# Kernel tuning notes

Hardware: AMD Instinct MI355X
Metric: run time of the kernel (lower is better)

## Reference

```python
import jax, jax.numpy as jnp
import numpy as np

DIM, ATT, G, T, KL, B = 1024, 128, 8, 4096, 256, 8
GD = DIM // G
SCALE = 1.0 / np.sqrt(ATT)

def setup_inputs() -> dict:
    key = jax.random.key(0)
    ks = jax.random.split(key, 7)
    x = jax.random.normal(ks[0], (B, T, DIM), dtype=jnp.float32)
    # stacked per-group weights (einsum orientation: in_dim x out_dim)
    Wq = jax.random.normal(ks[1], (G, GD, ATT), dtype=jnp.float32) * (1.0 / np.sqrt(GD))
    Wk = jax.random.normal(ks[2], (G, GD, ATT), dtype=jnp.float32) * (1.0 / np.sqrt(GD))
    Wv = jax.random.normal(ks[3], (G, GD, GD), dtype=jnp.float32) * (1.0 / np.sqrt(GD))
    Wo = jax.random.normal(ks[4], (G, GD, GD), dtype=jnp.float32) * (1.0 / np.sqrt(GD))
    Pk = jax.random.normal(ks[5], (G, T, KL), dtype=jnp.float32) * (1.0 / np.sqrt(T))
    Pv = jax.random.normal(ks[6], (G, T, KL), dtype=jnp.float32) * (1.0 / np.sqrt(T))
    return {"x": x, "Wq": Wq, "Wk": Wk, "Wv": Wv, "Wo": Wo, "Pk": Pk, "Pv": Pv}

def reference(x, Wq, Wk, Wv, Wo, Pk, Pv):
    Bx, Tx, _ = x.shape
    xg = x.reshape(Bx, Tx, G, GD).transpose(0, 2, 1, 3)        # [B,G,T,gd]
    q = jnp.einsum('bgtd,gda->bgta', xg, Wq)                   # [B,G,T,att]
    k = jnp.einsum('bgtd,gda->bgta', xg, Wk)
    v = jnp.einsum('bgtd,gde->bgte', xg, Wv)                   # [B,G,T,gd]
    k_red = jnp.einsum('bgta,gtk->bgka', k, Pk)                # [B,G,kl,att]
    v_red = jnp.einsum('bgte,gtk->bgke', v, Pv)                # [B,G,kl,gd]
    att = jax.nn.softmax(jnp.einsum('bgta,bgka->bgtk', q, k_red) * SCALE, axis=-1)
    out = jnp.einsum('bgtk,bgke->bgte', att, v_red)            # [B,G,T,gd]
    out = jnp.einsum('bgte,gef->bgtf', out, Wo)                # per-group output proj
    return out.transpose(0, 2, 1, 3).reshape(Bx, Tx, DIM)      # concat groups on last dim
```

## Files before the change

### kernel.cpp

```cpp
#include <hip/hip_runtime.h>
#include <hip/hip_bf16.h>

#define NB 8
#define NG 8
#define NT 4096
#define NDIM 1024
#define NGD 128
#define NATT 128
#define NKL 256
#define FSCALE 0.08838834764831845f

typedef __bf16 bf16x8 __attribute__((ext_vector_type(8)));
typedef float f32x4 __attribute__((ext_vector_type(4)));
typedef ushort u16x8 __attribute__((ext_vector_type(8)));
typedef ushort u16x4 __attribute__((ext_vector_type(4)));

#define MFMA(a, b, c) __builtin_amdgcn_mfma_f32_16x16x32_bf16(a, b, c, 0, 0, 0)

__device__ __forceinline__ ushort f2bf(float f) {
  union { float f; unsigned u; } v; v.f = f;
  unsigned r = v.u + 0x7FFFu + ((v.u >> 16) & 1u);
  return (ushort)(r >> 16);
}

__device__ __forceinline__ void gload16(const ushort* g, ushort* l) {
  __builtin_amdgcn_global_load_lds(
      (const __attribute__((address_space(1))) unsigned int*)g,
      (__attribute__((address_space(3))) unsigned int*)l, 16, 0, 0);
}

__global__ __launch_bounds__(512) void k0_weights(
    const float* __restrict__ Wq, const float* __restrict__ Wk,
    const float* __restrict__ Wv, const float* __restrict__ Wo,
    ushort* __restrict__ WkQT, ushort* __restrict__ WvoT) {
  const int sel = blockIdx.x;
  const int g = blockIdx.y;
  __shared__ float A2[128 * 136];
  __shared__ float B2[128 * 136];
  const int tid = threadIdx.x;

  if (sel == 0) {
#pragma unroll
    for (int u = 0; u < 8; ++u) {
      const int c = tid + 512 * u;
      const int row = c >> 5, c4 = (c & 31) * 4;
      *(float4*)&A2[row * 136 + c4] =
          *(const float4*)&Wo[(size_t)g * 16384 + row * 128 + c4];
      const float4 v = *(const float4*)&Wv[(size_t)g * 16384 + row * 128 + c4];
      B2[(c4 + 0) * 136 + row] = v.x;
      B2[(c4 + 1) * 136 + row] = v.y;
      B2[(c4 + 2) * 136 + row] = v.z;
      B2[(c4 + 3) * 136 + row] = v.w;
    }
  } else {
#pragma unroll
    for (int u = 0; u < 8; ++u) {
      const int c = tid + 512 * u;
      const int row = c >> 5, c4 = (c & 31) * 4;
      const float4 q = *(const float4*)&Wq[(size_t)g * 16384 + row * 128 + c4];
      A2[(c4 + 0) * 136 + row] = q.x;
      A2[(c4 + 1) * 136 + row] = q.y;
      A2[(c4 + 2) * 136 + row] = q.z;
      A2[(c4 + 3) * 136 + row] = q.w;
      const float4 k = *(const float4*)&Wk[(size_t)g * 16384 + row * 128 + c4];
      B2[(c4 + 0) * 136 + row] = k.x;
      B2[(c4 + 1) * 136 + row] = k.y;
      B2[(c4 + 2) * 136 + row] = k.z;
      B2[(c4 + 3) * 136 + row] = k.w;
    }
  }
  __syncthreads();

  const int mr = tid >> 4;
  const int mc = tid & 15;
  float acc[4][8];
#pragma unroll
  for (int i = 0; i < 4; ++i)
#pragma unroll
    for (int j = 0; j < 8; ++j) acc[i][j] = 0.f;

#pragma unroll 4
  for (int k = 0; k < 128; ++k) {
    const float4 a = *(const float4*)&A2[k * 136 + mr * 4];
    const float4 b0 = *(const float4*)&B2[k * 136 + mc * 8];
    const float4 b1 = *(const float4*)&B2[k * 136 + mc * 8 + 4];
    const float av[4] = {a.x, a.y, a.z, a.w};
    const float bv[8] = {b0.x, b0.y, b0.z, b0.w, b1.x, b1.y, b1.z, b1.w};
#pragma unroll
    for (int i = 0; i < 4; ++i)
#pragma unroll
      for (int j = 0; j < 8; ++j) acc[i][j] += av[i] * bv[j];
  }

  const float sc = sel ? FSCALE : 1.f;
  ushort* dst = (sel ? WkQT : WvoT) + (size_t)g * 16384;
#pragma unroll
  for (int i = 0; i < 4; ++i) {
    u16x8 pk;
#pragma unroll
    for (int j = 0; j < 8; ++j) pk[j] = f2bf(acc[i][j] * sc);
    *(u16x8*)&dst[(size_t)(mr * 4 + i) * 128 + mc * 8] = pk;
  }
}

__global__ __launch_bounds__(256) void kt_x(const float* __restrict__ x,
                                            ushort* __restrict__ xT) {
  const int t0 = blockIdx.x * 64;
  const int bg = blockIdx.y;
  const int b = bg >> 3, g = bg & 7;
  __shared__ float xl[64 * 132];
#pragma unroll
  for (int u = 0; u < 8; ++u) {
    const int c = threadIdx.x + 256 * u;
    const int row = c >> 5, c4 = (c & 31) * 4;
    *(float4*)&xl[row * 132 + c4] =
        *(const float4*)&x[((size_t)b * NT + t0 + row) * NDIM + g * 128 + c4];
  }
  __syncthreads();
  const int seg = threadIdx.x & 7;
  const int d0 = threadIdx.x >> 3;
#pragma unroll
  for (int u = 0; u < 4; ++u) {
    const int d = d0 + u * 32;
    u16x8 pk;
#pragma unroll
    for (int z = 0; z < 8; ++z) pk[z] = f2bf(xl[(seg * 8 + z) * 132 + d]);
    *(u16x8*)&xT[((size_t)bg * 128 + d) * NT + t0 + seg * 8] = pk;
  }
}

__global__ __launch_bounds__(256) void kt_p(const float* __restrict__ P,
                                            ushort* __restrict__ PT) {
  const int t0 = blockIdx.x * 64;
  const int klh = blockIdx.y, g = blockIdx.z;
  __shared__ float pl[64 * 132];
#pragma unroll
  for (int u = 0; u < 8; ++u) {
    const int c = threadIdx.x + 256 * u;
    const int row = c >> 5, c4 = (c & 31) * 4;
    *(float4*)&pl[row * 132 + c4] =
        *(const float4*)&P[((size_t)g * NT + t0 + row) * NKL + klh * 128 + c4];
  }
  __syncthreads();
  const int seg = threadIdx.x & 7;
  const int k0 = threadIdx.x >> 3;
#pragma unroll
  for (int u = 0; u < 4; ++u) {
    const int kl = k0 + u * 32;
    u16x8 pk;
#pragma unroll
    for (int z = 0; z < 8; ++z) pk[z] = f2bf(pl[(seg * 8 + z) * 132 + kl]);
    *(u16x8*)&PT[((size_t)g * NKL + klh * 128 + kl) * NT + t0 + seg * 8] = pk;
  }
}

__global__ __launch_bounds__(256, 2) void k1_mfma(
    const ushort* __restrict__ PkT, const ushort* __restrict__ PvT,
    const ushort* __restrict__ xT, const ushort* __restrict__ WkQT,
    const ushort* __restrict__ WvoT, ushort* __restrict__ MQ,
    ushort* __restrict__ vo_redT) {
  const int bid = blockIdx.x;
  const int work = (bid & 7) * 32 + (bid >> 3);
  const int bg = work >> 2;
  const int sel = (work >> 1) & 1;
  const int klt = work & 1;
  const int g = bg & 7;
  const ushort* PT = (sel ? PvT : PkT) + ((size_t)g * NKL + klt * 128) * NT;
  const ushort* Xb = xT + (size_t)bg * 128 * NT;

  __shared__ ushort lds[17408];

  const int tid = threadIdx.x;
  const int w = tid >> 6, lane = tid & 63;
  const int l15 = lane & 15, l4 = lane >> 4;
  const int rh = (w & 1) * 64;
  const int ch = (w >> 1) * 64;
  const int srow = lane >> 2, sc = lane & 3;

  f32x4 acc[4][4];
  const f32x4 fz = {0.f, 0.f, 0.f, 0.f};
#pragma unroll
  for (int i = 0; i < 4; ++i)
#pragma unroll
    for (int j = 0; j < 4; ++j) acc[i][j] = fz;

#define K1_STAGE(buf, s)                                                     \
  {                                                                          \
    const int t0_ = (s) * 32;                                                \
    ushort* Ab_ = &lds[(buf) * 8192];                                        \
    ushort* Bb_ = &lds[(buf) * 8192 + 4096];                                 \
    _Pragma("unroll") for (int u = 0; u < 2; ++u) {                          \
      const int row_ = w * 32 + u * 16 + srow;                               \
      const size_t off_ = (size_t)row_ * NT + t0_ + ((sc ^ (row_ & 3)) << 3);\
      gload16(PT + off_, Ab_ + (w * 32 + u * 16) * 32);                      \
      gload16(Xb + off_, Bb_ + (w * 32 + u * 16) * 32);                      \
    }                                                                        \
  }

#define K1_COMPUTE(buf)                                                      \
  {                                                                          \
    const ushort* Ab_ = &lds[(buf) * 8192];                                  \
    const ushort* Bb_ = &lds[(buf) * 8192 + 4096];                           \
    bf16x8 af_[4], bf_[4];                                                   \
    _Pragma("unroll") for (int i = 0; i < 4; ++i) {                          \
      const int row_ = rh + i * 16 + l15;                                    \
      af_[i] = *(const bf16x8*)&Ab_[row_ * 32 + ((l4 ^ (row_ & 3)) << 3)];   \
    }                                                                        \
    _Pragma("unroll") for (int j = 0; j < 4; ++j) {                          \
      const int row_ = ch + j * 16 + l15;                                    \
      bf_[j] = *(const bf16x8*)&Bb_[row_ * 32 + ((l4 ^ (row_ & 3)) << 3)];   \
    }                                                                        \
    _Pragma("unroll") for (int i = 0; i < 4; ++i)                            \
      _Pragma("unroll") for (int j = 0; j < 4; ++j)                          \
        acc[i][j] = MFMA(af_[i], bf_[j], acc[i][j]);                         \
  }

  K1_STAGE(0, 0);
  __syncthreads();
  int buf = 0;
#pragma unroll 1
  for (int s = 0; s < 128; ++s) {
    if (s + 1 < 128) K1_STAGE(buf ^ 1, s + 1);
    K1_COMPUTE(buf);
    __syncthreads();
    buf ^= 1;
  }

  ushort* C = lds;
#pragma unroll
  for (int i = 0; i < 4; ++i)
#pragma unroll
    for (int j = 0; j < 4; ++j)
#pragma unroll
      for (int r = 0; r < 4; ++r)
        C[(rh + i * 16 + l4 * 4 + r) * 136 + ch + j * 16 + l15] =
            f2bf(acc[i][j][r]);
  __syncthreads();

  const ushort* WT = (sel ? WvoT : WkQT) + (size_t)g * 16384;
  f32x4 o[4][4];
#pragma unroll
  for (int i = 0; i < 4; ++i)
#pragma unroll
    for (int j = 0; j < 4; ++j) o[i][j] = fz;
#pragma unroll
  for (int ks = 0; ks < 4; ++ks) {
    bf16x8 af[4], bfr[4];
#pragma unroll
    for (int i = 0; i < 4; ++i)
      af[i] = *(const bf16x8*)&C[(rh + i * 16 + l15) * 136 + ks * 32 + l4 * 8];
#pragma unroll
    for (int j = 0; j < 4; ++j)
      bfr[j] = *(const bf16x8*)&WT[(size_t)(ch + j * 16 + l15) * 128 + ks * 32 + l4 * 8];
#pragma unroll
    for (int i = 0; i < 4; ++i)
#pragma unroll
      for (int j = 0; j < 4; ++j) o[i][j] = MFMA(af[i], bfr[j], o[i][j]);
  }

  if (sel == 0) {
#pragma unroll
    for (int i = 0; i < 4; ++i)
#pragma unroll
      for (int j = 0; j < 4; ++j)
#pragma unroll
        for (int r = 0; r < 4; ++r)
          MQ[((size_t)bg * NKL + klt * 128 + rh + i * 16 + l4 * 4 + r) * 128 +
             ch + j * 16 + l15] = f2bf(o[i][j][r]);
  } else {
#pragma unroll
    for (int i = 0; i < 4; ++i)
#pragma unroll
      for (int j = 0; j < 4; ++j) {
        u16x4 pk;
#pragma unroll
        for (int r = 0; r < 4; ++r) pk[r] = f2bf(o[i][j][r]);
        *(u16x4*)&vo_redT[((size_t)bg * 128 + ch + j * 16 + l15) * NKL +
                          klt * 128 + rh + i * 16 + l4 * 4] = pk;
      }
  }
}

__global__ __launch_bounds__(512, 2) void k2_attn(
    const float* __restrict__ x, const ushort* __restrict__ MQ,
    const ushort* __restrict__ vo_redT, float* __restrict__ out) {
  const int tc = blockIdx.x;
  const int bg = blockIdx.y;
  const int b = bg >> 3, g = bg & 7;

  __shared__ ushort mq[256 * 136];
  __shared__ ushort att[64 * 264];
  __shared__ float redm[2][64];
  __shared__ float reds[2][64];

  const int tid = threadIdx.x;
  const int w = tid >> 6, lane = tid & 63;
  const int l15 = lane & 15, l4 = lane >> 4;
  const int tw = w >> 1, half = w & 1;
  const f32x4 fz = {0.f, 0.f, 0.f, 0.f};

  {
    const ushort* src = MQ + (size_t)bg * NKL * 128;
#pragma unroll
    for (int u = 0; u < 8; ++u) {
      const int c = tid + 512 * u;
      const int r = c >> 4, c8 = (c & 15) * 8;
      *(u16x8*)&mq[r * 136 + c8] = *(const u16x8*)&src[r * 128 + c8];
    }
  }

  const float* xb = x + ((size_t)b * NT + tc * 512) * NDIM + g * 128;
  const ushort* vo = vo_redT + ((size_t)bg * 128 + half * 64) * NKL;

  float4 xr[8];
#pragma unroll
  for (int ks = 0; ks < 4; ++ks) {
    const float* p = xb + (size_t)(tw * 16 + l15) * NDIM + ks * 32 + l4 * 8;
    xr[ks * 2] = *(const float4*)p;
    xr[ks * 2 + 1] = *(const float4*)(p + 4);
  }
  __syncthreads();

#pragma unroll 1
  for (int st = 0; st < 8; ++st) {
    bf16x8 a[4];
#pragma unroll
    for (int ks = 0; ks < 4; ++ks) {
      bf16x8 t;
      t[0] = (__bf16)xr[ks * 2].x; t[1] = (__bf16)xr[ks * 2].y;
      t[2] = (__bf16)xr[ks * 2].z; t[3] = (__bf16)xr[ks * 2].w;
      t[4] = (__bf16)xr[ks * 2 + 1].x; t[5] = (__bf16)xr[ks * 2 + 1].y;
      t[6] = (__bf16)xr[ks * 2 + 1].z; t[7] = (__bf16)xr[ks * 2 + 1].w;
      a[ks] = t;
    }
    if (st + 1 < 8) {
      const float* pn = xb + (size_t)((st + 1) * 64 + tw * 16 + l15) * NDIM;
#pragma unroll
      for (int ks = 0; ks < 4; ++ks) {
        xr[ks * 2] = *(const float4*)(pn + ks * 32 + l4 * 8);
        xr[ks * 2 + 1] = *(const float4*)(pn + ks * 32 + l4 * 8 + 4);
      }
    }
    f32x4 s[8];
#pragma unroll
    for (int n = 0; n < 8; ++n) s[n] = fz;
#pragma unroll
    for (int n = 0; n < 8; ++n) {
      const int row = (half * 8 + n) * 16 + l15;
#pragma unroll
      for (int ks = 0; ks < 4; ++ks) {
        const bf16x8 bv = *(const bf16x8*)&mq[row * 136 + ks * 32 + l4 * 8];
        s[n] = MFMA(a[ks], bv, s[n]);
      }
    }
    const int rowbase = tw * 16 + l4 * 4;
    float inv[4];
    {
      float mx[4];
#pragma unroll
      for (int r = 0; r < 4; ++r) {
        float m = s[0][r];
#pragma unroll
        for (int n = 1; n < 8; ++n) m = fmaxf(m, s[n][r]);
#pragma unroll
        for (int off = 1; off < 16; off <<= 1) m = fmaxf(m, __shfl_xor(m, off, 64));
        mx[r] = m;
      }
      if (l15 == 0) {
#pragma unroll
        for (int r = 0; r < 4; ++r) redm[half][rowbase + r] = mx[r];
      }
      __syncthreads();
      float sm[4];
#pragma unroll
      for (int r = 0; r < 4; ++r) {
        const float mg = fmaxf(mx[r], redm[half ^ 1][rowbase + r]);
        float acc = 0.f;
#pragma unroll
        for (int n = 0; n < 8; ++n) {
          const float p = __expf(s[n][r] - mg);
          acc += p;
          att[(rowbase + r) * 264 + (half * 8 + n) * 16 + l15] = f2bf(p);
        }
#pragma unroll
        for (int off = 1; off < 16; off <<= 1) acc += __shfl_xor(acc, off, 64);
        sm[r] = acc;
      }
      if (l15 == 0) {
#pragma unroll
        for (int r = 0; r < 4; ++r) reds[half][rowbase + r] = sm[r];
      }
      __syncthreads();
#pragma unroll
      for (int r = 0; r < 4; ++r)
        inv[r] = 1.f / (sm[r] + reds[half ^ 1][rowbase + r]);
    }
    f32x4 oa[4];
#pragma unroll
    for (int j = 0; j < 4; ++j) oa[j] = fz;
#pragma unroll
    for (int ks = 0; ks < 8; ++ks) {
      const bf16x8 av = *(const bf16x8*)&att[(tw * 16 + l15) * 264 + ks * 32 + l4 * 8];
#pragma unroll
      for (int j = 0; j < 4; ++j) {
        const bf16x8 bv = *(const bf16x8*)&vo[(size_t)(j * 16 + l15) * NKL + ks * 32 + l4 * 8];
        oa[j] = MFMA(av, bv, oa[j]);
      }
    }
    float* ob = out + ((size_t)b * NT + tc * 512 + st * 64 + tw * 16) * NDIM +
                g * 128 + half * 64;
#pragma unroll
    for (int j = 0; j < 4; ++j)
#pragma unroll
      for (int r = 0; r < 4; ++r)
        ob[(size_t)(l4 * 4 + r) * NDIM + j * 16 + l15] = oa[j][r] * inv[r];
  }
}

extern "C" void kernel_launch(void* const* d_in, const int* in_sizes, int n_in,
                              void* d_out, int out_size, void* d_ws, size_t ws_size,
                              hipStream_t stream) {
  (void)in_sizes; (void)n_in; (void)out_size; (void)ws_size;
  const float* x  = (const float*)d_in[0];
  const float* Wq = (const float*)d_in[1];
  const float* Wk = (const float*)d_in[2];
  const float* Wv = (const float*)d_in[3];
  const float* Wo = (const float*)d_in[4];
  const float* Pk = (const float*)d_in[5];
  const float* Pv = (const float*)d_in[6];

  ushort* wsu = (ushort*)d_ws;
  ushort* PkT     = wsu;
  ushort* PvT     = PkT + 8388608;
  ushort* WkQT    = PvT + 8388608;
  ushort* WvoT    = WkQT + 131072;
  ushort* MQ      = WvoT + 131072;
  ushort* vo_redT = MQ + 2097152;
  ushort* xT = (ushort*)d_out;

  k0_weights<<<dim3(2, NG), dim3(512), 0, stream>>>(Wq, Wk, Wv, Wo, WkQT, WvoT);
  kt_x<<<dim3(64, 64), dim3(256), 0, stream>>>(x, xT);
  kt_p<<<dim3(64, 2, 8), dim3(256), 0, stream>>>(Pk, PkT);
  kt_p<<<dim3(64, 2, 8), dim3(256), 0, stream>>>(Pv, PvT);
  k1_mfma<<<dim3(256), dim3(256), 0, stream>>>(PkT, PvT, xT, WkQT, WvoT,
                                               MQ, vo_redT);
  k2_attn<<<dim3(8, 64), dim3(512), 0, stream>>>(x, MQ, vo_redT, (float*)d_out);
}
```

Baseline: 259.6 us.

## Merge transpose kernels into one launch and deepen k1 K-tile to 64

The three transpose/convert kernels for x, Pk and Pv are merged into a single launch that dispatches on block index, removing two launches and their tail gaps. The k1 MFMA GEMM stage doubles its K-step from 32 to 64 per LDS buffer with an 8-way XOR swizzle, halving the number of barriers and loop iterations. The cost is that LDS per block roughly doubles to 64KB, which may limit the two-blocks-per-CU occupancy that launch_bounds requests.

```diff
diff --git a/kernel.cpp b/kernel.cpp
--- a/kernel.cpp
+++ b/kernel.cpp
@@ -103,54 +103,62 @@
   }
 }
 
-__global__ __launch_bounds__(256) void kt_x(const float* __restrict__ x,
-                                            ushort* __restrict__ xT) {
-  const int t0 = blockIdx.x * 64;
-  const int bg = blockIdx.y;
-  const int b = bg >> 3, g = bg & 7;
-  __shared__ float xl[64 * 132];
-#pragma unroll
-  for (int u = 0; u < 8; ++u) {
-    const int c = threadIdx.x + 256 * u;
-    const int row = c >> 5, c4 = (c & 31) * 4;
-    *(float4*)&xl[row * 132 + c4] =
-        *(const float4*)&x[((size_t)b * NT + t0 + row) * NDIM + g * 128 + c4];
-  }
-  __syncthreads();
-  const int seg = threadIdx.x & 7;
-  const int d0 = threadIdx.x >> 3;
-#pragma unroll
-  for (int u = 0; u < 4; ++u) {
-    const int d = d0 + u * 32;
-    u16x8 pk;
-#pragma unroll
-    for (int z = 0; z < 8; ++z) pk[z] = f2bf(xl[(seg * 8 + z) * 132 + d]);
-    *(u16x8*)&xT[((size_t)bg * 128 + d) * NT + t0 + seg * 8] = pk;
-  }
-}
-
-__global__ __launch_bounds__(256) void kt_p(const float* __restrict__ P,
-                                            ushort* __restrict__ PT) {
-  const int t0 = blockIdx.x * 64;
-  const int klh = blockIdx.y, g = blockIdx.z;
-  __shared__ float pl[64 * 132];
-#pragma unroll
-  for (int u = 0; u < 8; ++u) {
-    const int c = threadIdx.x + 256 * u;
-    const int row = c >> 5, c4 = (c & 31) * 4;
-    *(float4*)&pl[row * 132 + c4] =
-        *(const float4*)&P[((size_t)g * NT + t0 + row) * NKL + klh * 128 + c4];
-  }
-  __syncthreads();
-  const int seg = threadIdx.x & 7;
-  const int k0 = threadIdx.x >> 3;
-#pragma unroll
-  for (int u = 0; u < 4; ++u) {
-    const int kl = k0 + u * 32;
-    u16x8 pk;
-#pragma unroll
-    for (int z = 0; z < 8; ++z) pk[z] = f2bf(pl[(seg * 8 + z) * 132 + kl]);
-    *(u16x8*)&PT[((size_t)g * NKL + klh * 128 + kl) * NT + t0 + seg * 8] = pk;
+__global__ __launch_bounds__(256) void kt_xp(
+    const float* __restrict__ x, const float* __restrict__ Pk,
+    const float* __restrict__ Pv, ushort* __restrict__ xT,
+    ushort* __restrict__ PkT, ushort* __restrict__ PvT) {
+  __shared__ float buf[64 * 132];
+  const int bid = blockIdx.x;
+  const int tid = threadIdx.x;
+
+  if (bid < 4096) {
+    const int t0 = (bid & 63) * 64;
+    const int bg = bid >> 6;
+    const int b = bg >> 3, g = bg & 7;
+#pragma unroll
+    for (int u = 0; u < 8; ++u) {
+      const int c = tid + 256 * u;
+      const int row = c >> 5, c4 = (c & 31) * 4;
+      *(float4*)&buf[row * 132 + c4] =
+          *(const float4*)&x[((size_t)b * NT + t0 + row) * NDIM + g * 128 + c4];
+    }
+    __syncthreads();
+    const int seg = tid & 7;
+    const int d0 = tid >> 3;
+#pragma unroll
+    for (int u = 0; u < 4; ++u) {
+      const int d = d0 + u * 32;
+      u16x8 pk;
+#pragma unroll
+      for (int z = 0; z < 8; ++z) pk[z] = f2bf(buf[(seg * 8 + z) * 132 + d]);
+      *(u16x8*)&xT[((size_t)bg * 128 + d) * NT + t0 + seg * 8] = pk;
+    }
+  } else {
+    const int idx = bid - 4096;
+    const float* P = (idx >> 10) ? Pv : Pk;
+    ushort* PT = (idx >> 10) ? PvT : PkT;
+    const int r_ = idx & 1023;
+    const int t0 = (r_ & 63) * 64;
+    const int klh = (r_ >> 6) & 1;
+    const int g = (r_ >> 7) & 7;
+#pragma unroll
+    for (int u = 0; u < 8; ++u) {
+      const int c = tid + 256 * u;
+      const int row = c >> 5, c4 = (c & 31) * 4;
+      *(float4*)&buf[row * 132 + c4] =
+          *(const float4*)&P[((size_t)g * NT + t0 + row) * NKL + klh * 128 + c4];
+    }
+    __syncthreads();
+    const int seg = tid & 7;
+    const int k0_ = tid >> 3;
+#pragma unroll
+    for (int u = 0; u < 4; ++u) {
+      const int kl = k0_ + u * 32;
+      u16x8 pk;
+#pragma unroll
+      for (int z = 0; z < 8; ++z) pk[z] = f2bf(buf[(seg * 8 + z) * 132 + kl]);
+      *(u16x8*)&PT[((size_t)g * NKL + klh * 128 + kl) * NT + t0 + seg * 8] = pk;
+    }
   }
 }
 
@@ -168,14 +176,14 @@
   const ushort* PT = (sel ? PvT : PkT) + ((size_t)g * NKL + klt * 128) * NT;
   const ushort* Xb = xT + (size_t)bg * 128 * NT;
 
-  __shared__ ushort lds[17408];
+  __shared__ ushort lds[32768];
 
   const int tid = threadIdx.x;
   const int w = tid >> 6, lane = tid & 63;
   const int l15 = lane & 15, l4 = lane >> 4;
   const int rh = (w & 1) * 64;
   const int ch = (w >> 1) * 64;
-  const int srow = lane >> 2, sc = lane & 3;
+  const int srow = lane >> 3, sc = lane & 7;
 
   f32x4 acc[4][4];
   const f32x4 fz = {0.f, 0.f, 0.f, 0.f};
@@ -184,43 +192,47 @@
 #pragma unroll
     for (int j = 0; j < 4; ++j) acc[i][j] = fz;
 
-#define K1_STAGE(buf, s)                                                     \
-  {                                                                          \
-    const int t0_ = (s) * 32;                                                \
-    ushort* Ab_ = &lds[(buf) * 8192];                                        \
-    ushort* Bb_ = &lds[(buf) * 8192 + 4096];                                 \
-    _Pragma("unroll") for (int u = 0; u < 2; ++u) {                          \
-      const int row_ = w * 32 + u * 16 + srow;                               \
-      const size_t off_ = (size_t)row_ * NT + t0_ + ((sc ^ (row_ & 3)) << 3);\
-      gload16(PT + off_, Ab_ + (w * 32 + u * 16) * 32);                      \
-      gload16(Xb + off_, Bb_ + (w * 32 + u * 16) * 32);                      \
-    }                                                                        \
-  }
-
-#define K1_COMPUTE(buf)                                                      \
-  {                                                                          \
-    const ushort* Ab_ = &lds[(buf) * 8192];                                  \
-    const ushort* Bb_ = &lds[(buf) * 8192 + 4096];                           \
-    bf16x8 af_[4], bf_[4];                                                   \
-    _Pragma("unroll") for (int i = 0; i < 4; ++i) {                          \
-      const int row_ = rh + i * 16 + l15;                                    \
-      af_[i] = *(const bf16x8*)&Ab_[row_ * 32 + ((l4 ^ (row_ & 3)) << 3)];   \
-    }                                                                        \
-    _Pragma("unroll") for (int j = 0; j < 4; ++j) {                          \
-      const int row_ = ch + j * 16 + l15;                                    \
-      bf_[j] = *(const bf16x8*)&Bb_[row_ * 32 + ((l4 ^ (row_ & 3)) << 3)];   \
-    }                                                                        \
-    _Pragma("unroll") for (int i = 0; i < 4; ++i)                            \
-      _Pragma("unroll") for (int j = 0; j < 4; ++j)                          \
-        acc[i][j] = MFMA(af_[i], bf_[j], acc[i][j]);                         \
+#define K1_STAGE(buf, s)                                                      \
+  {                                                                           \
+    const int t0_ = (s) * 64;                                                 \
+    ushort* Ab_ = &lds[(buf) * 16384];                                        \
+    ushort* Bb_ = &lds[(buf) * 16384 + 8192];                                 \
+    _Pragma("unroll") for (int u = 0; u < 4; ++u) {                           \
+      const int row_ = w * 32 + u * 8 + srow;                                 \
+      const size_t off_ = (size_t)row_ * NT + t0_ + ((sc ^ (row_ & 7)) << 3); \
+      gload16(PT + off_, Ab_ + (w * 32 + u * 8) * 64);                        \
+      gload16(Xb + off_, Bb_ + (w * 32 + u * 8) * 64);                        \
+    }                                                                         \
+  }
+
+#define K1_COMPUTE(buf)                                                       \
+  {                                                                           \
+    const ushort* Ab_ = &lds[(buf) * 16384];                                  \
+    const ushort* Bb_ = &lds[(buf) * 16384 + 8192];                           \
+    _Pragma("unroll") for (int h = 0; h < 2; ++h) {                           \
+      bf16x8 af_[4], bf_[4];                                                  \
+      _Pragma("unroll") for (int i = 0; i < 4; ++i) {                         \
+        const int row_ = rh + i * 16 + l15;                                   \
+        af_[i] = *(const bf16x8*)&Ab_[row_ * 64 +                             \
+                                      (((h * 4 + l4) ^ (row_ & 7)) << 3)];    \
+      }                                                                       \
+      _Pragma("unroll") for (int j = 0; j < 4; ++j) {                         \
+        const int row_ = ch + j * 16 + l15;                                   \
+        bf_[j] = *(const bf16x8*)&Bb_[row_ * 64 +                             \
+                                      (((h * 4 + l4) ^ (row_ & 7)) << 3)];    \
+      }                                                                       \
+      _Pragma("unroll") for (int i = 0; i < 4; ++i)                           \
+        _Pragma("unroll") for (int j = 0; j < 4; ++j)                         \
+          acc[i][j] = MFMA(af_[i], bf_[j], acc[i][j]);                        \
+    }                                                                         \
   }
 
   K1_STAGE(0, 0);
   __syncthreads();
   int buf = 0;
 #pragma unroll 1
-  for (int s = 0; s < 128; ++s) {
-    if (s + 1 < 128) K1_STAGE(buf ^ 1, s + 1);
+  for (int s = 0; s < 64; ++s) {
+    if (s + 1 < 64) K1_STAGE(buf ^ 1, s + 1);
     K1_COMPUTE(buf);
     __syncthreads();
     buf ^= 1;
@@ -439,9 +451,7 @@
   ushort* xT = (ushort*)d_out;
 
   k0_weights<<<dim3(2, NG), dim3(512), 0, stream>>>(Wq, Wk, Wv, Wo, WkQT, WvoT);
-  kt_x<<<dim3(64, 64), dim3(256), 0, stream>>>(x, xT);
-  kt_p<<<dim3(64, 2, 8), dim3(256), 0, stream>>>(Pk, PkT);
-  kt_p<<<dim3(64, 2, 8), dim3(256), 0, stream>>>(Pv, PvT);
+  kt_xp<<<dim3(4096 + 2048), dim3(256), 0, stream>>>(x, Pk, Pv, xT, PkT, PvT);
   k1_mfma<<<dim3(256), dim3(256), 0, stream>>>(PkT, PvT, xT, WkQT, WvoT,
                                                MQ, vo_redT);
   k2_attn<<<dim3(8, 64), dim3(512), 0, stream>>>(x, MQ, vo_redT, (float*)d_out);
```

Measured after the change: 242.7 us. 6.5% less time.
